# Kernel tuning notes

Hardware: AMD Instinct MI355X
Metric: run time of the kernel (lower is better)

## Reference

```python
import jax, jax.numpy as jnp
import numpy as np

EPS = 1e-05


def setup_inputs() -> dict:
    key = jax.random.key(0)
    k1, k2, k3, k4, k5 = jax.random.split(key, 5)
    B, Cin, T = 8, 512, 4096
    K, N, D = 8, 2048, 256
    return {
        "embeddings": jax.random.normal(k1, (B, Cin, T), dtype=jnp.float32),
        "w_in": jax.random.normal(k2, (D, Cin), dtype=jnp.float32) * 0.05,
        "w_out": jax.random.normal(k3, (Cin, D), dtype=jnp.float32) * 0.05,
        "embed_sum": jax.random.normal(k4, (K, N, D), dtype=jnp.float32),
        "cluster_usage": jax.random.uniform(k5, (K, N), dtype=jnp.float32, minval=0.5, maxval=1.5),
    }


def reference(embeddings, w_in, w_out, embed_sum, cluster_usage):
    # input_proj: 1x1 conv == channel matmul. [B, 512, T] -> [B, T, 256]
    x = jnp.einsum("dc,bct->btd", w_in, embeddings)
    # per-quantizer codebooks: embed_sum / clamp(cluster_usage)  -> [K, N, D]
    embeds = embed_sum / jnp.clip(cluster_usage, EPS, None)[..., None]

    def step(residual, embed):
        # squared-euclidean distance (same argmin as cdist p=2)
        # dists: [B, T, N]
        d = (
            jnp.sum(residual * residual, axis=-1, keepdims=True)
            - 2.0 * jnp.einsum("btd,nd->btn", residual, embed)
            + jnp.sum(embed * embed, axis=-1)
        )
        idx = jnp.argmin(d, axis=-1)          # [B, T] int
        q = embed[idx]                        # gather -> [B, T, D]
        return residual - q, (idx, q)

    _, (codes, qs) = jax.lax.scan(step, x, embeds)
    # codes: [K, B, T]; qs: [K, B, T, D]
    quantized = jnp.sum(qs, axis=0)           # decode: sum over quantizers
    out = jnp.einsum("cd,btd->bct", w_out, quantized)  # output_proj -> [B, 512, T]
    return codes, out
```

## Files before the change

kernel.cpp:

```cpp
#include <hip/hip_runtime.h>
#include <float.h>
#include <math.h>

#define EPSF 1e-5f
#define NRM_BIAS 2048.0f

constexpr int B_  = 8;
constexpr int CIN = 512;
constexpr int T_  = 4096;
constexpr int K_  = 8;
constexpr int N_  = 2048;
constexpr int D_  = 256;
constexpr int BT  = B_ * T_;

typedef _Float16 v8h __attribute__((ext_vector_type(8)));
typedef _Float16 v4h __attribute__((ext_vector_type(4)));
typedef float    v4f __attribute__((ext_vector_type(4)));

static __device__ __forceinline__ unsigned umn(unsigned a, unsigned b) { return a < b ? a : b; }
static __device__ __forceinline__ unsigned umx(unsigned a, unsigned b) { return a > b ? a : b; }

__global__ void __launch_bounds__(256) prep_kernel(const float* __restrict__ embed_sum,
                                                   const float* __restrict__ usage,
                                                   float* __restrict__ inv,
                                                   float* __restrict__ nrm,
                                                   _Float16* __restrict__ ehs) {
  int w    = threadIdx.x >> 6;
  int lane = threadIdx.x & 63;
  int kn   = blockIdx.x * 4 + w;
  int k    = kn >> 11, n = kn & (N_ - 1);
  const float* s = embed_sum + (size_t)kn * D_;
  float um = fmaxf(usage[kn], EPSF);
  float4 sv = *(const float4*)(s + lane * 4);
  float e0 = sv.x / um, e1 = sv.y / um, e2 = sv.z / um, e3 = sv.w / um;
  float v = e0 * e0 + e1 * e1 + e2 * e2 + e3 * e3;

  int half = n >> 10, chunk = (n >> 4) & 63, r = n & 15;
  int cg = lane >> 1, sub = lane & 1;
  v4h h4; h4[0] = (_Float16)e0; h4[1] = (_Float16)e1;
  h4[2] = (_Float16)e2; h4[3] = (_Float16)e3;
  size_t off16 = ((size_t)((k * 2 + half) * 64 + chunk)) * 4096
               + (size_t)(cg * 16 + r) * 8 + (size_t)sub * 4;
  *(v4h*)(ehs + off16) = h4;

  for (int off = 32; off > 0; off >>= 1) v += __shfl_down(v, off);
  if (lane == 0) { inv[kn] = 1.0f / um; nrm[kn] = v + NRM_BIAS; }
}

__global__ void __launch_bounds__(64) wprep_x_kernel(const float* __restrict__ w_in,
                                                     v8h* __restrict__ afragX) {
  int lane = threadIdx.x;
  int mt = blockIdx.x >> 4, kstep = blockIdx.x & 15;
  int m = mt * 16 + (lane & 15), k0 = kstep * 32 + (lane >> 4) * 8;
  const float* src = w_in + (size_t)m * CIN + k0;
  float4 f0 = *(const float4*)src, f1 = *(const float4*)(src + 4);
  float e[8] = {f0.x, f0.y, f0.z, f0.w, f1.x, f1.y, f1.z, f1.w};
  v8h h, l;
#pragma unroll
  for (int j = 0; j < 8; j++) {
    _Float16 hh = (_Float16)e[j];
    h[j] = hh; l[j] = (_Float16)(e[j] - (float)hh);
  }
  v8h* dst = afragX + ((size_t)blockIdx.x * 64 + lane) * 2;
  dst[0] = h; dst[1] = l;
}

__global__ void __launch_bounds__(256) wc_kernel(const float* __restrict__ w_out,
                                                 const float* __restrict__ w_in,
                                                 float* __restrict__ wc) {
  int c  = blockIdx.x >> 1;
  int cp = (blockIdx.x & 1) * 256 + threadIdx.x;
  float acc = 0.f;
  for (int d = 0; d < D_; d++)
    acc += w_out[(size_t)c * D_ + d] * w_in[(size_t)d * CIN + cp];
  wc[(size_t)c * CIN + cp] = acc;
}

__global__ void __launch_bounds__(64) wprep_o_kernel(const float* __restrict__ wc,
                                                     const float* __restrict__ w_out,
                                                     v8h* __restrict__ afragO) {
  int lane = threadIdx.x;
  int mt = blockIdx.x / 24, kstep = blockIdx.x % 24;
  int m = mt * 16 + (lane & 15), k0 = kstep * 32 + (lane >> 4) * 8;
  float e[8];
  if (k0 < CIN) {
    const float* s = wc + (size_t)m * CIN + k0;
#pragma unroll
    for (int j = 0; j < 8; j++) e[j] = s[j];
  } else {
    const float* s = w_out + (size_t)m * D_ + (k0 - CIN);
#pragma unroll
    for (int j = 0; j < 8; j++) e[j] = -s[j];
  }
  v8h h, l;
#pragma unroll
  for (int j = 0; j < 8; j++) {
    _Float16 hh = (_Float16)e[j];
    h[j] = hh; l[j] = (_Float16)(e[j] - (float)hh);
  }
  v8h* dst = afragO + ((size_t)blockIdx.x * 64 + lane) * 2;
  dst[0] = h; dst[1] = l;
}

__global__ void __launch_bounds__(256, 4) proj_x_kernel(const float* __restrict__ emb,
                                                        const v8h* __restrict__ afragX,
                                                        float* __restrict__ rb) {
  int tid = threadIdx.x, wave = tid >> 6, lane = tid & 63;
  int lr = lane & 15, lg = lane >> 4;
  int tb = blockIdx.x >> 1, nb = blockIdx.x & 1;
  int t0 = tb * 64 + wave * 16;
  int b  = t0 >> 12;
  const float* ebase = emb + (size_t)b * CIN * T_ + (t0 & (T_ - 1)) + lr;

  v4f acc[8];
#pragma unroll
  for (int nt = 0; nt < 8; nt++) acc[nt] = (v4f){0.f, 0.f, 0.f, 0.f};

  for (int ks = 0; ks < 16; ks++) {
    float e[8];
#pragma unroll
    for (int j = 0; j < 8; j++)
      e[j] = ebase[(size_t)(ks * 32 + lg * 8 + j) * T_];
    v8h Eh, El;
#pragma unroll
    for (int j = 0; j < 8; j++) {
      _Float16 hh = (_Float16)e[j];
      Eh[j] = hh; El[j] = (_Float16)(e[j] - (float)hh);
    }
    const v8h* ap = afragX + ((size_t)ks * 64 + lane) * 2;
#pragma unroll
    for (int nt = 0; nt < 8; nt++) {
      int mt = nb * 8 + nt;
      v8h Wh = ap[(size_t)mt * 2048];
      v8h Wl = ap[(size_t)mt * 2048 + 1];
      acc[nt] = __builtin_amdgcn_mfma_f32_16x16x32_f16(Eh, Wh, acc[nt], 0, 0, 0);
      acc[nt] = __builtin_amdgcn_mfma_f32_16x16x32_f16(El, Wh, acc[nt], 0, 0, 0);
      acc[nt] = __builtin_amdgcn_mfma_f32_16x16x32_f16(Eh, Wl, acc[nt], 0, 0, 0);
    }
  }
#pragma unroll
  for (int nt = 0; nt < 8; nt++)
#pragma unroll
    for (int r = 0; r < 4; r++)
      rb[(size_t)(t0 + lg * 4 + r) * D_ + (nb * 8 + nt) * 16 + lr] = acc[nt][r];
}

__global__ void __launch_bounds__(256, 4) proj_out_kernel(const float* __restrict__ emb,
                                                          const float* __restrict__ rb,
                                                          const v8h* __restrict__ afragO,
                                                          float* __restrict__ outb) {
  int tid = threadIdx.x, wave = tid >> 6, lane = tid & 63;
  int lr = lane & 15, lg = lane >> 4;
  int tb = blockIdx.x >> 1, mb = blockIdx.x & 1;
  int t0 = tb * 64 + wave * 16;
  int b  = t0 >> 12;
  const float* ebase = emb + (size_t)b * CIN * T_ + (t0 & (T_ - 1)) + lr;

  v4f acc[16];
#pragma unroll
  for (int mt = 0; mt < 16; mt++) acc[mt] = (v4f){0.f, 0.f, 0.f, 0.f};

  for (int ks = 0; ks < 24; ks++) {
    float e[8];
    if (ks < 16) {
#pragma unroll
      for (int j = 0; j < 8; j++)
        e[j] = ebase[(size_t)(ks * 32 + lg * 8 + j) * T_];
    } else {
      const float* rrow = rb + (size_t)(t0 + lr) * D_ + (ks - 16) * 32 + lg * 8;
      float4 f0 = *(const float4*)rrow, f1 = *(const float4*)(rrow + 4);
      e[0] = f0.x; e[1] = f0.y; e[2] = f0.z; e[3] = f0.w;
      e[4] = f1.x; e[5] = f1.y; e[6] = f1.z; e[7] = f1.w;
    }
    v8h Bh;
#pragma unroll
    for (int j = 0; j < 8; j++) Bh[j] = (_Float16)e[j];
#pragma unroll
    for (int mt = 0; mt < 16; mt++) {
      v8h Ah = afragO[(((size_t)(mb * 16 + mt) * 24 + ks) * 64 + lane) * 2];
      acc[mt] = __builtin_amdgcn_mfma_f32_16x16x32_f16(Ah, Bh, acc[mt], 0, 0, 0);
    }
  }
  float* op = outb + (size_t)b * CIN * T_ + (t0 & (T_ - 1)) + lr;
#pragma unroll
  for (int mt = 0; mt < 16; mt++)
#pragma unroll
    for (int r = 0; r < 4; r++)
      op[(size_t)((mb * 16 + mt) * 16 + lg * 4 + r) * T_] = acc[mt][r];
}

__device__ __forceinline__ void merge_save(unsigned b1[4], unsigned b2[4], unsigned b3[4],
                                           int half, int wave, int lg, int lr,
                                           int (*candL)[6]) {
#pragma unroll
  for (int rI = 0; rI < 4; rI++) {
    unsigned k1 = b1[rI], k2 = b2[rI], k3 = b3[rI];
    int n1 = (int)(k1 & 127u) * 16 + lr;
    int n2 = (int)(k2 & 127u) * 16 + lr;
    int n3 = (int)(k3 & 127u) * 16 + lr;
    int o0 = 0, o1 = 0, o2v = 0;
#pragma unroll
    for (int round = 0; round < 3; round++) {
      unsigned mk = k1; int mn = n1;
#pragma unroll
      for (int st = 1; st < 16; st <<= 1) {
        unsigned ok = (unsigned)__shfl_xor((int)mk, st);
        int      on = __shfl_xor(mn, st);
        bool t = (ok < mk) || (ok == mk && on < mn);
        mk = t ? ok : mk; mn = t ? on : mn;
      }
      if (round == 0) o0 = mn; else if (round == 1) o1 = mn; else o2v = mn;
      bool own = (k1 == mk) && (n1 == mn);
      k1 = own ? k2 : k1; n1 = own ? n2 : n1;
      k2 = own ? k3 : k2; n2 = own ? n3 : n2;
      k3 = own ? 0xFFFFFFFFu : k3; n3 = own ? 0x7fffffff : n3;
    }
    if (lr == 0) {
      int* cp = candL[wave * 16 + lg * 4 + rI] + half * 3;
      cp[0] = o0; cp[1] = o1; cp[2] = o2v;
    }
  }
}

__global__ void __launch_bounds__(512) rvq_fused_kernel(const _Float16* __restrict__ ehs,
                                                        const float* __restrict__ nrm,
                                                        const float* __restrict__ inv_,
                                                        const float* __restrict__ usage,
                                                        const float* __restrict__ embed_sum,
                                                        float* __restrict__ rb,
                                                        float* __restrict__ codes_f, int k) {
  __shared__ v8h ldsB[2][1024];
  __shared__ int candL[128][6];

  int tid  = threadIdx.x;
  int wave = tid >> 6, lane = tid & 63;
  int lr = lane & 15, lg = lane >> 4;
  int wbase = blockIdx.x * 128 + wave * 16;

  v8h A[8];
  {
    const float* rrow = rb + (size_t)(wbase + lr) * D_;
#pragma unroll
    for (int c = 0; c < 8; c++) {
      int k0 = c * 32 + lg * 8;
      float4 f0 = *(const float4*)(rrow + k0);
      float4 f1 = *(const float4*)(rrow + k0 + 4);
      v8h a;
      a[0] = (_Float16)f0.x; a[1] = (_Float16)f0.y;
      a[2] = (_Float16)f0.z; a[3] = (_Float16)f0.w;
      a[4] = (_Float16)f1.x; a[5] = (_Float16)f1.y;
      a[6] = (_Float16)f1.z; a[7] = (_Float16)f1.w;
      A[c] = a;
    }
  }

  const v8h* src = (const v8h*)(ehs + (size_t)k * 2 * (64 * 4096));
  ldsB[0][tid]       = src[tid];
  ldsB[0][512 + tid] = src[512 + tid];

  unsigned b1[4], b2[4], b3[4];
#pragma unroll
  for (int i = 0; i < 4; i++) { b1[i] = b2[i] = b3[i] = 0xFFFFFFFFu; }
  const float* nrm_k = nrm + (size_t)k * N_;
  __syncthreads();

  for (int p = 0; p < 64; p++) {
    int cur = p & 1;
    v8h nxt0, nxt1;
    bool more = (p + 1 < 64);
    if (more) {
      nxt0 = src[(size_t)(p + 1) * 1024 + tid];
      nxt1 = src[(size_t)(p + 1) * 1024 + 512 + tid];
    }

    v4f accA = {0.f, 0.f, 0.f, 0.f}, accB = {0.f, 0.f, 0.f, 0.f};
#pragma unroll
    for (int c = 0; c < 8; c++) {
      v8h BfA = ldsB[cur][(c * 4 + lg) * 16 + lr];
      v8h BfB = ldsB[cur][512 + (c * 4 + lg) * 16 + lr];
      accA = __builtin_amdgcn_mfma_f32_16x16x32_f16(A[c], BfA, accA, 0, 0, 0);
      accB = __builtin_amdgcn_mfma_f32_16x16x32_f16(A[c], BfB, accB, 0, 0, 0);
    }
    unsigned cgA = 2 * p, cgB = 2 * p + 1;
    float nvA = nrm_k[cgA * 16 + lr];
    float nvB = nrm_k[cgB * 16 + lr];
#pragma unroll
    for (int j = 0; j < 4; j++) {
      {
        float s = fmaf(-2.0f, accA[j], nvA);
        unsigned pk = (__float_as_uint(s) & 0xFFFFFF80u) | cgA;
        unsigned t = umx(b1[j], pk);
        unsigned u = umx(b2[j], pk);
        b1[j] = umn(b1[j], pk);
        b2[j] = umn(b2[j], t);
        b3[j] = umn(b3[j], u);
      }
      {
        float s = fmaf(-2.0f, accB[j], nvB);
        unsigned pk = (__float_as_uint(s) & 0xFFFFFF80u) | cgB;
        unsigned t = umx(b1[j], pk);
        unsigned u = umx(b2[j], pk);
        b1[j] = umn(b1[j], pk);
        b2[j] = umn(b2[j], t);
        b3[j] = umn(b3[j], u);
      }
    }
    if (more) {
      ldsB[cur ^ 1][tid]       = nxt0;
      ldsB[cur ^ 1][512 + tid] = nxt1;
    }
    if (p == 31) {
      merge_save(b1, b2, b3, 0, wave, lg, lr, candL);
#pragma unroll
      for (int i = 0; i < 4; i++) { b1[i] = b2[i] = b3[i] = 0xFFFFFFFFu; }
    }
    __syncthreads();
  }
  merge_save(b1, b2, b3, 1, wave, lg, lr, candL);
  __syncthreads();

  int tt = tid >> 2, q = tid & 3;
  int token = blockIdx.x * 128 + tt;
  const float* es_k  = embed_sum + (size_t)k * N_ * D_;
  const float* us_k  = usage + (size_t)k * N_;
  const float* inv_k = inv_  + (size_t)k * N_;

  int c6[6];
#pragma unroll
  for (int i = 0; i < 6; i++) c6[i] = candL[tt][i];
  float* rrow = rb + (size_t)token * D_;
  float* rq = rrow + q * 64;
  float4 rv[16];
#pragma unroll
  for (int m = 0; m < 16; m++) rv[m] = *(const float4*)(rq + m * 4);

  float dots[6];
#pragma unroll
  for (int i = 0; i < 6; i++) {
    const float* sr = es_k + (size_t)c6[i] * D_ + q * 64;
    float a = 0.f;
#pragma unroll
    for (int m = 0; m < 16; m++) {
      float4 sv = *(const float4*)(sr + m * 4);
      a += rv[m].x * sv.x + rv[m].y * sv.y + rv[m].z * sv.z + rv[m].w * sv.w;
    }
    dots[i] = a;
  }
#pragma unroll
  for (int st = 1; st < 4; st <<= 1) {
#pragma unroll
    for (int i = 0; i < 6; i++) dots[i] += __shfl_xor(dots[i], st);
  }

  float bs = FLT_MAX, bv2 = FLT_MAX; int bn = 0x7fffffff, bn2 = 0x7fffffff;
#pragma unroll
  for (int i = 0; i < 6; i++) {
    int n = c6[i];
    float s = nrm_k[n] - 2.0f * inv_k[n] * dots[i];
    bool better = (s < bs) || (s == bs && n < bn);
    bool second = (s < bv2) || (s == bv2 && n < bn2);
    if (better)      { bv2 = bs; bn2 = bn; bs = s; bn = n; }
    else if (second) { bv2 = s;  bn2 = n; }
  }
  int winner = bn;
  if (bv2 - bs < 0.5f && bn2 != bn) {
    double sc[2]; int nn[2] = { bn, bn2 };
#pragma unroll
    for (int cI = 0; cI < 2; cI++) {
      double u = fmax((double)us_k[nn[cI]], 1e-5);
      double uinv = 1.0 / u;
      const float* srow = es_k + (size_t)nn[cI] * D_ + q * 64;
      double dotre = 0.0, ee = 0.0;
#pragma unroll
      for (int m = 0; m < 16; m++) {
        float4 sv = *(const float4*)(srow + m * 4);
        double e0 = (double)sv.x * uinv, e1 = (double)sv.y * uinv;
        double e2 = (double)sv.z * uinv, e3 = (double)sv.w * uinv;
        dotre += (double)rv[m].x * e0 + (double)rv[m].y * e1
               + (double)rv[m].z * e2 + (double)rv[m].w * e3;
        ee += e0 * e0 + e1 * e1 + e2 * e2 + e3 * e3;
      }
      dotre += __shfl_xor(dotre, 1); dotre += __shfl_xor(dotre, 2);
      ee    += __shfl_xor(ee, 1);    ee    += __shfl_xor(ee, 2);
      sc[cI] = ee - 2.0 * dotre;
    }
    if (sc[1] < sc[0] || (sc[1] == sc[0] && nn[1] < nn[0])) winner = nn[1];
  }

  float um = fmaxf(us_k[winner], EPSF);
  const float* sw = es_k + (size_t)winner * D_ + q * 64;
#pragma unroll
  for (int m = 0; m < 16; m++) {
    float4 sv = *(const float4*)(sw + m * 4);
    rv[m].x -= sv.x / um; rv[m].y -= sv.y / um;
    rv[m].z -= sv.z / um; rv[m].w -= sv.w / um;
    *(float4*)(rq + m * 4) = rv[m];
  }
  if (q == 0) codes_f[(size_t)k * BT + token] = (float)winner;
}

extern "C" void kernel_launch(void* const* d_in, const int* in_sizes, int n_in,
                              void* d_out, int out_size, void* d_ws, size_t ws_size,
                              hipStream_t stream) {
  const float* emb       = (const float*)d_in[0];
  const float* w_in      = (const float*)d_in[1];
  const float* w_out     = (const float*)d_in[2];
  const float* embed_sum = (const float*)d_in[3];
  const float* usage     = (const float*)d_in[4];

  float* outp    = (float*)d_out;
  float* codes_f = outp;
  float* proj_o  = outp + (size_t)K_ * BT;

  float* rb   = (float*)d_ws;
  float* inv  = rb + (size_t)BT * D_;
  float* nrm  = inv + (size_t)K_ * N_;
  int*   cand = (int*)(nrm + (size_t)K_ * N_);
  _Float16* ehs = (_Float16*)(cand + (size_t)BT * 6);
  v8h* afragX = (v8h*)(ehs + (size_t)K_ * N_ * D_);
  float* wc   = (float*)(afragX + 16 * 16 * 64 * 2);
  v8h* afragO = (v8h*)(wc + 512 * 512);

  hipLaunchKernelGGL(wprep_x_kernel, dim3(256), dim3(64), 0, stream, w_in, afragX);
  hipLaunchKernelGGL(wc_kernel, dim3(1024), dim3(256), 0, stream, w_out, w_in, wc);
  hipLaunchKernelGGL(wprep_o_kernel, dim3(768), dim3(64), 0, stream, wc, w_out, afragO);
  hipLaunchKernelGGL(prep_kernel, dim3(K_ * N_ / 4), dim3(256), 0, stream,
                     embed_sum, usage, inv, nrm, ehs);
  hipLaunchKernelGGL(proj_x_kernel, dim3(BT / 32), dim3(256), 0, stream,
                     emb, afragX, rb);
  for (int k = 0; k < K_; k++)
    hipLaunchKernelGGL(rvq_fused_kernel, dim3(BT / 128), dim3(512), 0, stream,
                       ehs, nrm, inv, usage, embed_sum, rb, codes_f, k);
  hipLaunchKernelGGL(proj_out_kernel, dim3(BT / 32), dim3(256), 0, stream,
                     emb, rb, afragO, proj_o);
}
```

Before: 997.4 us.

## Fuse all eight quantizer stages into one kernel with register-resident residual

Replaces the eight per-quantizer launches with a single kernel that loops over quantizers, keeping each token's residual in registers (64 floats per lane) instead of reloading and storing it through global memory at every stage. The refinement and residual-update phase is remapped so that the same lanes that own the MFMA A-fragment own the residual slice, with cross-lane reductions over lane groups. The intent is to remove per-stage launch overhead and residual global-memory round trips. The cost is higher register pressure from the 64-float array, which the launch bound of two blocks per CU is meant to accommodate.

Measured after the change: 894.1 us. 1.12x faster.

```diff
diff --git a/kernel.cpp b/kernel.cpp
--- a/kernel.cpp
+++ b/kernel.cpp
@@ -222,13 +222,13 @@
   }
 }
 
-__global__ void __launch_bounds__(512) rvq_fused_kernel(const _Float16* __restrict__ ehs,
-                                                        const float* __restrict__ nrm,
-                                                        const float* __restrict__ inv_,
-                                                        const float* __restrict__ usage,
-                                                        const float* __restrict__ embed_sum,
-                                                        float* __restrict__ rb,
-                                                        float* __restrict__ codes_f, int k) {
+__global__ void __launch_bounds__(512, 2) rvq_mega_kernel(const _Float16* __restrict__ ehs,
+                                                          const float* __restrict__ nrm,
+                                                          const float* __restrict__ inv_,
+                                                          const float* __restrict__ usage,
+                                                          const float* __restrict__ embed_sum,
+                                                          float* __restrict__ rb,
+                                                          float* __restrict__ codes_f) {
   __shared__ v8h ldsB[2][1024];
   __shared__ int candL[128][6];
 
@@ -236,167 +236,194 @@
   int wave = tid >> 6, lane = tid & 63;
   int lr = lane & 15, lg = lane >> 4;
   int wbase = blockIdx.x * 128 + wave * 16;
-
-  v8h A[8];
+  int token = wbase + lr;
+
+  float r64[64];
   {
-    const float* rrow = rb + (size_t)(wbase + lr) * D_;
+    const float* rrow = rb + (size_t)token * D_ + lg * 8;
 #pragma unroll
     for (int c = 0; c < 8; c++) {
-      int k0 = c * 32 + lg * 8;
-      float4 f0 = *(const float4*)(rrow + k0);
-      float4 f1 = *(const float4*)(rrow + k0 + 4);
+      float4 f0 = *(const float4*)(rrow + c * 32);
+      float4 f1 = *(const float4*)(rrow + c * 32 + 4);
+      r64[c * 8 + 0] = f0.x; r64[c * 8 + 1] = f0.y;
+      r64[c * 8 + 2] = f0.z; r64[c * 8 + 3] = f0.w;
+      r64[c * 8 + 4] = f1.x; r64[c * 8 + 5] = f1.y;
+      r64[c * 8 + 6] = f1.z; r64[c * 8 + 7] = f1.w;
+    }
+  }
+
+  for (int k = 0; k < K_; k++) {
+    v8h A[8];
+#pragma unroll
+    for (int c = 0; c < 8; c++) {
       v8h a;
-      a[0] = (_Float16)f0.x; a[1] = (_Float16)f0.y;
-      a[2] = (_Float16)f0.z; a[3] = (_Float16)f0.w;
-      a[4] = (_Float16)f1.x; a[5] = (_Float16)f1.y;
-      a[6] = (_Float16)f1.z; a[7] = (_Float16)f1.w;
+#pragma unroll
+      for (int j = 0; j < 8; j++) a[j] = (_Float16)r64[c * 8 + j];
       A[c] = a;
     }
-  }
-
-  const v8h* src = (const v8h*)(ehs + (size_t)k * 2 * (64 * 4096));
-  ldsB[0][tid]       = src[tid];
-  ldsB[0][512 + tid] = src[512 + tid];
-
-  unsigned b1[4], b2[4], b3[4];
-#pragma unroll
-  for (int i = 0; i < 4; i++) { b1[i] = b2[i] = b3[i] = 0xFFFFFFFFu; }
-  const float* nrm_k = nrm + (size_t)k * N_;
-  __syncthreads();
-
-  for (int p = 0; p < 64; p++) {
-    int cur = p & 1;
-    v8h nxt0, nxt1;
-    bool more = (p + 1 < 64);
-    if (more) {
-      nxt0 = src[(size_t)(p + 1) * 1024 + tid];
-      nxt1 = src[(size_t)(p + 1) * 1024 + 512 + tid];
-    }
-
-    v4f accA = {0.f, 0.f, 0.f, 0.f}, accB = {0.f, 0.f, 0.f, 0.f};
+
+    const v8h* src = (const v8h*)(ehs + (size_t)k * 2 * (64 * 4096));
+    ldsB[0][tid]       = src[tid];
+    ldsB[0][512 + tid] = src[512 + tid];
+
+    unsigned b1[4], b2[4], b3[4];
+#pragma unroll
+    for (int i = 0; i < 4; i++) { b1[i] = b2[i] = b3[i] = 0xFFFFFFFFu; }
+    const float* nrm_k = nrm + (size_t)k * N_;
+    __syncthreads();
+
+    for (int p = 0; p < 64; p++) {
+      int cur = p & 1;
+      v8h nxt0, nxt1;
+      bool more = (p + 1 < 64);
+      if (more) {
+        nxt0 = src[(size_t)(p + 1) * 1024 + tid];
+        nxt1 = src[(size_t)(p + 1) * 1024 + 512 + tid];
+      }
+
+      v4f accA = {0.f, 0.f, 0.f, 0.f}, accB = {0.f, 0.f, 0.f, 0.f};
+#pragma unroll
+      for (int c = 0; c < 8; c++) {
+        v8h BfA = ldsB[cur][(c * 4 + lg) * 16 + lr];
+        v8h BfB = ldsB[cur][512 + (c * 4 + lg) * 16 + lr];
+        accA = __builtin_amdgcn_mfma_f32_16x16x32_f16(A[c], BfA, accA, 0, 0, 0);
+        accB = __builtin_amdgcn_mfma_f32_16x16x32_f16(A[c], BfB, accB, 0, 0, 0);
+      }
+      unsigned cgA = 2 * p, cgB = 2 * p + 1;
+      float nvA = nrm_k[cgA * 16 + lr];
+      float nvB = nrm_k[cgB * 16 + lr];
+#pragma unroll
+      for (int j = 0; j < 4; j++) {
+        {
+          float s = fmaf(-2.0f, accA[j], nvA);
+          unsigned pk = (__float_as_uint(s) & 0xFFFFFF80u) | cgA;
+          unsigned t = umx(b1[j], pk);
+          unsigned u = umx(b2[j], pk);
+          b1[j] = umn(b1[j], pk);
+          b2[j] = umn(b2[j], t);
+          b3[j] = umn(b3[j], u);
+        }
+        {
+          float s = fmaf(-2.0f, accB[j], nvB);
+          unsigned pk = (__float_as_uint(s) & 0xFFFFFF80u) | cgB;
+          unsigned t = umx(b1[j], pk);
+          unsigned u = umx(b2[j], pk);
+          b1[j] = umn(b1[j], pk);
+          b2[j] = umn(b2[j], t);
+          b3[j] = umn(b3[j], u);
+        }
+      }
+      if (more) {
+        ldsB[cur ^ 1][tid]       = nxt0;
+        ldsB[cur ^ 1][512 + tid] = nxt1;
+      }
+      if (p == 31) {
+        merge_save(b1, b2, b3, 0, wave, lg, lr, candL);
+#pragma unroll
+        for (int i = 0; i < 4; i++) { b1[i] = b2[i] = b3[i] = 0xFFFFFFFFu; }
+      }
+      __syncthreads();
+    }
+    merge_save(b1, b2, b3, 1, wave, lg, lr, candL);
+    __syncthreads();
+
+    const float* es_k  = embed_sum + (size_t)k * N_ * D_;
+    const float* us_k  = usage + (size_t)k * N_;
+    const float* inv_k = inv_  + (size_t)k * N_;
+
+    int c6[6];
+#pragma unroll
+    for (int i = 0; i < 6; i++) c6[i] = candL[wave * 16 + lr][i];
+
+    float dots[6];
+#pragma unroll
+    for (int i = 0; i < 6; i++) {
+      const float* sr = es_k + (size_t)c6[i] * D_ + lg * 8;
+      float a = 0.f;
+#pragma unroll
+      for (int c = 0; c < 8; c++) {
+        float4 s0 = *(const float4*)(sr + c * 32);
+        float4 s1 = *(const float4*)(sr + c * 32 + 4);
+        a += r64[c * 8 + 0] * s0.x + r64[c * 8 + 1] * s0.y
+           + r64[c * 8 + 2] * s0.z + r64[c * 8 + 3] * s0.w
+           + r64[c * 8 + 4] * s1.x + r64[c * 8 + 5] * s1.y
+           + r64[c * 8 + 6] * s1.z + r64[c * 8 + 7] * s1.w;
+      }
+      dots[i] = a;
+    }
+#pragma unroll
+    for (int i = 0; i < 6; i++) {
+      dots[i] += __shfl_xor(dots[i], 16);
+      dots[i] += __shfl_xor(dots[i], 32);
+    }
+
+    float bs = FLT_MAX, bv2 = FLT_MAX; int bn = 0x7fffffff, bn2 = 0x7fffffff;
+#pragma unroll
+    for (int i = 0; i < 6; i++) {
+      int n = c6[i];
+      float s = nrm_k[n] - 2.0f * inv_k[n] * dots[i];
+      bool better = (s < bs) || (s == bs && n < bn);
+      bool second = (s < bv2) || (s == bv2 && n < bn2);
+      if (better)      { bv2 = bs; bn2 = bn; bs = s; bn = n; }
+      else if (second) { bv2 = s;  bn2 = n; }
+    }
+    int winner = bn;
+    if (bv2 - bs < 0.5f && bn2 != bn) {
+      double sc[2]; int nn[2] = { bn, bn2 };
+#pragma unroll
+      for (int cI = 0; cI < 2; cI++) {
+        double u = fmax((double)us_k[nn[cI]], 1e-5);
+        double uinv = 1.0 / u;
+        const float* srow = es_k + (size_t)nn[cI] * D_ + lg * 8;
+        double dotre = 0.0, ee = 0.0;
+#pragma unroll
+        for (int c = 0; c < 8; c++) {
+          float4 s0 = *(const float4*)(srow + c * 32);
+          float4 s1 = *(const float4*)(srow + c * 32 + 4);
+          double e0 = (double)s0.x * uinv, e1 = (double)s0.y * uinv;
+          double e2 = (double)s0.z * uinv, e3 = (double)s0.w * uinv;
+          double e4 = (double)s1.x * uinv, e5 = (double)s1.y * uinv;
+          double e6 = (double)s1.z * uinv, e7 = (double)s1.w * uinv;
+          dotre += (double)r64[c * 8 + 0] * e0 + (double)r64[c * 8 + 1] * e1
+                 + (double)r64[c * 8 + 2] * e2 + (double)r64[c * 8 + 3] * e3
+                 + (double)r64[c * 8 + 4] * e4 + (double)r64[c * 8 + 5] * e5
+                 + (double)r64[c * 8 + 6] * e6 + (double)r64[c * 8 + 7] * e7;
+          ee += e0 * e0 + e1 * e1 + e2 * e2 + e3 * e3
+              + e4 * e4 + e5 * e5 + e6 * e6 + e7 * e7;
+        }
+        dotre += __shfl_xor(dotre, 16); dotre += __shfl_xor(dotre, 32);
+        ee    += __shfl_xor(ee, 16);    ee    += __shfl_xor(ee, 32);
+        sc[cI] = ee - 2.0 * dotre;
+      }
+      if (sc[1] < sc[0] || (sc[1] == sc[0] && nn[1] < nn[0])) winner = nn[1];
+    }
+
+    float um = fmaxf(us_k[winner], EPSF);
+    const float* sw = es_k + (size_t)winner * D_ + lg * 8;
 #pragma unroll
     for (int c = 0; c < 8; c++) {
-      v8h BfA = ldsB[cur][(c * 4 + lg) * 16 + lr];
-      v8h BfB = ldsB[cur][512 + (c * 4 + lg) * 16 + lr];
-      accA = __builtin_amdgcn_mfma_f32_16x16x32_f16(A[c], BfA, accA, 0, 0, 0);
-      accB = __builtin_amdgcn_mfma_f32_16x16x32_f16(A[c], BfB, accB, 0, 0, 0);
-    }
-    unsigned cgA = 2 * p, cgB = 2 * p + 1;
-    float nvA = nrm_k[cgA * 16 + lr];
-    float nvB = nrm_k[cgB * 16 + lr];
-#pragma unroll
-    for (int j = 0; j < 4; j++) {
-      {
-        float s = fmaf(-2.0f, accA[j], nvA);
-        unsigned pk = (__float_as_uint(s) & 0xFFFFFF80u) | cgA;
-        unsigned t = umx(b1[j], pk);
-        unsigned u = umx(b2[j], pk);
-        b1[j] = umn(b1[j], pk);
-        b2[j] = umn(b2[j], t);
-        b3[j] = umn(b3[j], u);
-      }
-      {
-        float s = fmaf(-2.0f, accB[j], nvB);
-        unsigned pk = (__float_as_uint(s) & 0xFFFFFF80u) | cgB;
-        unsigned t = umx(b1[j], pk);
-        unsigned u = umx(b2[j], pk);
-        b1[j] = umn(b1[j], pk);
-        b2[j] = umn(b2[j], t);
-        b3[j] = umn(b3[j], u);
-      }
-    }
-    if (more) {
-      ldsB[cur ^ 1][tid]       = nxt0;
-      ldsB[cur ^ 1][512 + tid] = nxt1;
-    }
-    if (p == 31) {
-      merge_save(b1, b2, b3, 0, wave, lg, lr, candL);
-#pragma unroll
-      for (int i = 0; i < 4; i++) { b1[i] = b2[i] = b3[i] = 0xFFFFFFFFu; }
-    }
-    __syncthreads();
-  }
-  merge_save(b1, b2, b3, 1, wave, lg, lr, candL);
-  __syncthreads();
-
-  int tt = tid >> 2, q = tid & 3;
-  int token = blockIdx.x * 128 + tt;
-  const float* es_k  = embed_sum + (size_t)k * N_ * D_;
-  const float* us_k  = usage + (size_t)k * N_;
-  const float* inv_k = inv_  + (size_t)k * N_;
-
-  int c6[6];
-#pragma unroll
-  for (int i = 0; i < 6; i++) c6[i] = candL[tt][i];
-  float* rrow = rb + (size_t)token * D_;
-  float* rq = rrow + q * 64;
-  float4 rv[16];
-#pragma unroll
-  for (int m = 0; m < 16; m++) rv[m] = *(const float4*)(rq + m * 4);
-
-  float dots[6];
-#pragma unroll
-  for (int i = 0; i < 6; i++) {
-    const float* sr = es_k + (size_t)c6[i] * D_ + q * 64;
-    float a = 0.f;
-#pragma unroll
-    for (int m = 0; m < 16; m++) {
-      float4 sv = *(const float4*)(sr + m * 4);
-      a += rv[m].x * sv.x + rv[m].y * sv.y + rv[m].z * sv.z + rv[m].w * sv.w;
-    }
-    dots[i] = a;
-  }
-#pragma unroll
-  for (int st = 1; st < 4; st <<= 1) {
-#pragma unroll
-    for (int i = 0; i < 6; i++) dots[i] += __shfl_xor(dots[i], st);
-  }
-
-  float bs = FLT_MAX, bv2 = FLT_MAX; int bn = 0x7fffffff, bn2 = 0x7fffffff;
-#pragma unroll
-  for (int i = 0; i < 6; i++) {
-    int n = c6[i];
-    float s = nrm_k[n] - 2.0f * inv_k[n] * dots[i];
-    bool better = (s < bs) || (s == bs && n < bn);
-    bool second = (s < bv2) || (s == bv2 && n < bn2);
-    if (better)      { bv2 = bs; bn2 = bn; bs = s; bn = n; }
-    else if (second) { bv2 = s;  bn2 = n; }
-  }
-  int winner = bn;
-  if (bv2 - bs < 0.5f && bn2 != bn) {
-    double sc[2]; int nn[2] = { bn, bn2 };
-#pragma unroll
-    for (int cI = 0; cI < 2; cI++) {
-      double u = fmax((double)us_k[nn[cI]], 1e-5);
-      double uinv = 1.0 / u;
-      const float* srow = es_k + (size_t)nn[cI] * D_ + q * 64;
-      double dotre = 0.0, ee = 0.0;
-#pragma unroll
-      for (int m = 0; m < 16; m++) {
-        float4 sv = *(const float4*)(srow + m * 4);
-        double e0 = (double)sv.x * uinv, e1 = (double)sv.y * uinv;
-        double e2 = (double)sv.z * uinv, e3 = (double)sv.w * uinv;
-        dotre += (double)rv[m].x * e0 + (double)rv[m].y * e1
-               + (double)rv[m].z * e2 + (double)rv[m].w * e3;
-        ee += e0 * e0 + e1 * e1 + e2 * e2 + e3 * e3;
-      }
-      dotre += __shfl_xor(dotre, 1); dotre += __shfl_xor(dotre, 2);
-      ee    += __shfl_xor(ee, 1);    ee    += __shfl_xor(ee, 2);
-      sc[cI] = ee - 2.0 * dotre;
-    }
-    if (sc[1] < sc[0] || (sc[1] == sc[0] && nn[1] < nn[0])) winner = nn[1];
-  }
-
-  float um = fmaxf(us_k[winner], EPSF);
-  const float* sw = es_k + (size_t)winner * D_ + q * 64;
-#pragma unroll
-  for (int m = 0; m < 16; m++) {
-    float4 sv = *(const float4*)(sw + m * 4);
-    rv[m].x -= sv.x / um; rv[m].y -= sv.y / um;
-    rv[m].z -= sv.z / um; rv[m].w -= sv.w / um;
-    *(float4*)(rq + m * 4) = rv[m];
-  }
-  if (q == 0) codes_f[(size_t)k * BT + token] = (float)winner;
+      float4 s0 = *(const float4*)(sw + c * 32);
+      float4 s1 = *(const float4*)(sw + c * 32 + 4);
+      r64[c * 8 + 0] -= s0.x / um; r64[c * 8 + 1] -= s0.y / um;
+      r64[c * 8 + 2] -= s0.z / um; r64[c * 8 + 3] -= s0.w / um;
+      r64[c * 8 + 4] -= s1.x / um; r64[c * 8 + 5] -= s1.y / um;
+      r64[c * 8 + 6] -= s1.z / um; r64[c * 8 + 7] -= s1.w / um;
+    }
+    if (lg == 0) codes_f[(size_t)k * BT + token] = (float)winner;
+  }
+
+  {
+    float* wrow = rb + (size_t)token * D_ + lg * 8;
+#pragma unroll
+    for (int c = 0; c < 8; c++) {
+      float4 f0 = make_float4(r64[c * 8 + 0], r64[c * 8 + 1],
+                              r64[c * 8 + 2], r64[c * 8 + 3]);
+      float4 f1 = make_float4(r64[c * 8 + 4], r64[c * 8 + 5],
+                              r64[c * 8 + 6], r64[c * 8 + 7]);
+      *(float4*)(wrow + c * 32)     = f0;
+      *(float4*)(wrow + c * 32 + 4) = f1;
+    }
+  }
 }
 
 extern "C" void kernel_launch(void* const* d_in, const int* in_sizes, int n_in,
@@ -428,9 +455,8 @@
                      embed_sum, usage, inv, nrm, ehs);
   hipLaunchKernelGGL(proj_x_kernel, dim3(BT / 32), dim3(256), 0, stream,
                      emb, afragX, rb);
-  for (int k = 0; k < K_; k++)
-    hipLaunchKernelGGL(rvq_fused_kernel, dim3(BT / 128), dim3(512), 0, stream,
-                       ehs, nrm, inv, usage, embed_sum, rb, codes_f, k);
+  hipLaunchKernelGGL(rvq_mega_kernel, dim3(BT / 128), dim3(512), 0, stream,
+                     ehs, nrm, inv, usage, embed_sum, rb, codes_f);
   hipLaunchKernelGGL(proj_out_kernel, dim3(BT / 32), dim3(256), 0, stream,
                      emb, rb, afragO, proj_o);
 }
```

## Fuse all quantizer stages into one persistent kernel with 32 tokens per wave

Applied to the files above, without the earlier changes.

Replaces the eight per-quantizer launches with a single kernel that loops over the quantizers. Each block still handles its own 128 tokens, and the residuals stay block-local from one stage to the next. Each wave now covers 32 tokens with two A-fragment sets, so every codebook tile read from LDS feeds twice as many MFMAs. Codebook tiles are staged with global_load_lds direct-to-LDS copies instead of register round-trips. The cost is half as many waves per block (256 threads), more registers for accumulators and top-3 lists, and a serial candidate-rescore phase done in two halves.

Measured after the change: 1.202 ms. 1.21x slower.

```diff
diff --git a/kernel.cpp b/kernel.cpp
--- a/kernel.cpp
+++ b/kernel.cpp
@@ -19,6 +19,15 @@
 
 static __device__ __forceinline__ unsigned umn(unsigned a, unsigned b) { return a < b ? a : b; }
 static __device__ __forceinline__ unsigned umx(unsigned a, unsigned b) { return a > b ? a : b; }
+
+static __device__ __forceinline__ void ins3(unsigned& B1, unsigned& B2, unsigned& B3,
+                                            unsigned pk) {
+  unsigned t = umx(B1, pk);
+  unsigned u = umx(B2, pk);
+  B1 = umn(B1, pk);
+  B2 = umn(B2, t);
+  B3 = umn(B3, u);
+}
 
 __global__ void __launch_bounds__(256) prep_kernel(const float* __restrict__ embed_sum,
                                                    const float* __restrict__ usage,
@@ -189,11 +198,11 @@
       op[(size_t)((mb * 16 + mt) * 16 + lg * 4 + r) * T_] = acc[mt][r];
 }
 
-__device__ __forceinline__ void merge_save(unsigned b1[4], unsigned b2[4], unsigned b3[4],
-                                           int half, int wave, int lg, int lr,
-                                           int (*candL)[6]) {
-#pragma unroll
-  for (int rI = 0; rI < 4; rI++) {
+__device__ __forceinline__ void merge_save8(unsigned b1[8], unsigned b2[8], unsigned b3[8],
+                                            int half, int wave, int lg, int lr,
+                                            int (*candL)[6]) {
+#pragma unroll
+  for (int rI = 0; rI < 8; rI++) {
     unsigned k1 = b1[rI], k2 = b2[rI], k3 = b3[rI];
     int n1 = (int)(k1 & 127u) * 16 + lr;
     int n2 = (int)(k2 & 127u) * 16 + lr;
@@ -216,187 +225,191 @@
       k3 = own ? 0xFFFFFFFFu : k3; n3 = own ? 0x7fffffff : n3;
     }
     if (lr == 0) {
-      int* cp = candL[wave * 16 + lg * 4 + rI] + half * 3;
+      int* cp = candL[wave * 32 + (rI >> 2) * 16 + lg * 4 + (rI & 3)] + half * 3;
       cp[0] = o0; cp[1] = o1; cp[2] = o2v;
     }
   }
 }
 
-__global__ void __launch_bounds__(512) rvq_fused_kernel(const _Float16* __restrict__ ehs,
-                                                        const float* __restrict__ nrm,
-                                                        const float* __restrict__ inv_,
-                                                        const float* __restrict__ usage,
-                                                        const float* __restrict__ embed_sum,
-                                                        float* __restrict__ rb,
-                                                        float* __restrict__ codes_f, int k) {
+__global__ void __launch_bounds__(256) rvq_mega_kernel(const _Float16* __restrict__ ehs,
+                                                       const float* __restrict__ nrm,
+                                                       const float* __restrict__ inv_,
+                                                       const float* __restrict__ usage,
+                                                       const float* __restrict__ embed_sum,
+                                                       float* __restrict__ rb,
+                                                       float* __restrict__ codes_f) {
   __shared__ v8h ldsB[2][1024];
   __shared__ int candL[128][6];
 
   int tid  = threadIdx.x;
   int wave = tid >> 6, lane = tid & 63;
   int lr = lane & 15, lg = lane >> 4;
-  int wbase = blockIdx.x * 128 + wave * 16;
-
-  v8h A[8];
-  {
-    const float* rrow = rb + (size_t)(wbase + lr) * D_;
-#pragma unroll
-    for (int c = 0; c < 8; c++) {
-      int k0 = c * 32 + lg * 8;
-      float4 f0 = *(const float4*)(rrow + k0);
-      float4 f1 = *(const float4*)(rrow + k0 + 4);
-      v8h a;
-      a[0] = (_Float16)f0.x; a[1] = (_Float16)f0.y;
-      a[2] = (_Float16)f0.z; a[3] = (_Float16)f0.w;
-      a[4] = (_Float16)f1.x; a[5] = (_Float16)f1.y;
-      a[6] = (_Float16)f1.z; a[7] = (_Float16)f1.w;
-      A[c] = a;
-    }
-  }
-
-  const v8h* src = (const v8h*)(ehs + (size_t)k * 2 * (64 * 4096));
-  ldsB[0][tid]       = src[tid];
-  ldsB[0][512 + tid] = src[512 + tid];
-
-  unsigned b1[4], b2[4], b3[4];
-#pragma unroll
-  for (int i = 0; i < 4; i++) { b1[i] = b2[i] = b3[i] = 0xFFFFFFFFu; }
-  const float* nrm_k = nrm + (size_t)k * N_;
-  __syncthreads();
-
-  for (int p = 0; p < 64; p++) {
-    int cur = p & 1;
-    v8h nxt0, nxt1;
-    bool more = (p + 1 < 64);
-    if (more) {
-      nxt0 = src[(size_t)(p + 1) * 1024 + tid];
-      nxt1 = src[(size_t)(p + 1) * 1024 + 512 + tid];
-    }
-
-    v4f accA = {0.f, 0.f, 0.f, 0.f}, accB = {0.f, 0.f, 0.f, 0.f};
-#pragma unroll
-    for (int c = 0; c < 8; c++) {
-      v8h BfA = ldsB[cur][(c * 4 + lg) * 16 + lr];
-      v8h BfB = ldsB[cur][512 + (c * 4 + lg) * 16 + lr];
-      accA = __builtin_amdgcn_mfma_f32_16x16x32_f16(A[c], BfA, accA, 0, 0, 0);
-      accB = __builtin_amdgcn_mfma_f32_16x16x32_f16(A[c], BfB, accB, 0, 0, 0);
-    }
-    unsigned cgA = 2 * p, cgB = 2 * p + 1;
-    float nvA = nrm_k[cgA * 16 + lr];
-    float nvB = nrm_k[cgB * 16 + lr];
-#pragma unroll
-    for (int j = 0; j < 4; j++) {
-      {
-        float s = fmaf(-2.0f, accA[j], nvA);
-        unsigned pk = (__float_as_uint(s) & 0xFFFFFF80u) | cgA;
-        unsigned t = umx(b1[j], pk);
-        unsigned u = umx(b2[j], pk);
-        b1[j] = umn(b1[j], pk);
-        b2[j] = umn(b2[j], t);
-        b3[j] = umn(b3[j], u);
-      }
-      {
-        float s = fmaf(-2.0f, accB[j], nvB);
-        unsigned pk = (__float_as_uint(s) & 0xFFFFFF80u) | cgB;
-        unsigned t = umx(b1[j], pk);
-        unsigned u = umx(b2[j], pk);
-        b1[j] = umn(b1[j], pk);
-        b2[j] = umn(b2[j], t);
-        b3[j] = umn(b3[j], u);
-      }
-    }
-    if (more) {
-      ldsB[cur ^ 1][tid]       = nxt0;
-      ldsB[cur ^ 1][512 + tid] = nxt1;
-    }
-    if (p == 31) {
-      merge_save(b1, b2, b3, 0, wave, lg, lr, candL);
-#pragma unroll
-      for (int i = 0; i < 4; i++) { b1[i] = b2[i] = b3[i] = 0xFFFFFFFFu; }
-    }
+  int wbase = blockIdx.x * 128 + wave * 32;
+
+  for (int k = 0; k < K_; k++) {
+    v8h A[2][8];
+#pragma unroll
+    for (int tau = 0; tau < 2; tau++) {
+      const float* rrow = rb + (size_t)(wbase + tau * 16 + lr) * D_ + lg * 8;
+#pragma unroll
+      for (int c = 0; c < 8; c++) {
+        float4 f0 = *(const float4*)(rrow + c * 32);
+        float4 f1 = *(const float4*)(rrow + c * 32 + 4);
+        v8h a;
+        a[0] = (_Float16)f0.x; a[1] = (_Float16)f0.y;
+        a[2] = (_Float16)f0.z; a[3] = (_Float16)f0.w;
+        a[4] = (_Float16)f1.x; a[5] = (_Float16)f1.y;
+        a[6] = (_Float16)f1.z; a[7] = (_Float16)f1.w;
+        A[tau][c] = a;
+      }
+    }
+
+    const v8h* src = (const v8h*)(ehs + (size_t)k * 2 * (64 * 4096));
+
+#pragma unroll
+    for (int q = 0; q < 4; q++) {
+      int idx = tid + q * 256;
+      __builtin_amdgcn_global_load_lds(
+          (__attribute__((address_space(1))) void*)(void*)(src + idx),
+          (__attribute__((address_space(3))) void*)(&ldsB[0][idx]), 16, 0, 0);
+    }
+
+    unsigned b1[8], b2[8], b3[8];
+#pragma unroll
+    for (int i = 0; i < 8; i++) { b1[i] = b2[i] = b3[i] = 0xFFFFFFFFu; }
+    const float* nrm_k = nrm + (size_t)k * N_;
     __syncthreads();
-  }
-  merge_save(b1, b2, b3, 1, wave, lg, lr, candL);
-  __syncthreads();
-
-  int tt = tid >> 2, q = tid & 3;
-  int token = blockIdx.x * 128 + tt;
-  const float* es_k  = embed_sum + (size_t)k * N_ * D_;
-  const float* us_k  = usage + (size_t)k * N_;
-  const float* inv_k = inv_  + (size_t)k * N_;
-
-  int c6[6];
-#pragma unroll
-  for (int i = 0; i < 6; i++) c6[i] = candL[tt][i];
-  float* rrow = rb + (size_t)token * D_;
-  float* rq = rrow + q * 64;
-  float4 rv[16];
-#pragma unroll
-  for (int m = 0; m < 16; m++) rv[m] = *(const float4*)(rq + m * 4);
-
-  float dots[6];
-#pragma unroll
-  for (int i = 0; i < 6; i++) {
-    const float* sr = es_k + (size_t)c6[i] * D_ + q * 64;
-    float a = 0.f;
-#pragma unroll
-    for (int m = 0; m < 16; m++) {
-      float4 sv = *(const float4*)(sr + m * 4);
-      a += rv[m].x * sv.x + rv[m].y * sv.y + rv[m].z * sv.z + rv[m].w * sv.w;
-    }
-    dots[i] = a;
-  }
-#pragma unroll
-  for (int st = 1; st < 4; st <<= 1) {
-#pragma unroll
-    for (int i = 0; i < 6; i++) dots[i] += __shfl_xor(dots[i], st);
-  }
-
-  float bs = FLT_MAX, bv2 = FLT_MAX; int bn = 0x7fffffff, bn2 = 0x7fffffff;
-#pragma unroll
-  for (int i = 0; i < 6; i++) {
-    int n = c6[i];
-    float s = nrm_k[n] - 2.0f * inv_k[n] * dots[i];
-    bool better = (s < bs) || (s == bs && n < bn);
-    bool second = (s < bv2) || (s == bv2 && n < bn2);
-    if (better)      { bv2 = bs; bn2 = bn; bs = s; bn = n; }
-    else if (second) { bv2 = s;  bn2 = n; }
-  }
-  int winner = bn;
-  if (bv2 - bs < 0.5f && bn2 != bn) {
-    double sc[2]; int nn[2] = { bn, bn2 };
-#pragma unroll
-    for (int cI = 0; cI < 2; cI++) {
-      double u = fmax((double)us_k[nn[cI]], 1e-5);
-      double uinv = 1.0 / u;
-      const float* srow = es_k + (size_t)nn[cI] * D_ + q * 64;
-      double dotre = 0.0, ee = 0.0;
+
+    for (int p = 0; p < 64; p++) {
+      int cur = p & 1;
+      if (p + 1 < 64) {
+        const v8h* gsrc = src + (size_t)(p + 1) * 1024;
+#pragma unroll
+        for (int q = 0; q < 4; q++) {
+          int idx = tid + q * 256;
+          __builtin_amdgcn_global_load_lds(
+              (__attribute__((address_space(1))) void*)(void*)(gsrc + idx),
+              (__attribute__((address_space(3))) void*)(&ldsB[cur ^ 1][idx]), 16, 0, 0);
+        }
+      }
+
+      v4f a0A = {0,0,0,0}, a0B = {0,0,0,0}, a1A = {0,0,0,0}, a1B = {0,0,0,0};
+#pragma unroll
+      for (int c = 0; c < 8; c++) {
+        v8h BfA = ldsB[cur][(c * 4 + lg) * 16 + lr];
+        v8h BfB = ldsB[cur][512 + (c * 4 + lg) * 16 + lr];
+        a0A = __builtin_amdgcn_mfma_f32_16x16x32_f16(A[0][c], BfA, a0A, 0, 0, 0);
+        a0B = __builtin_amdgcn_mfma_f32_16x16x32_f16(A[0][c], BfB, a0B, 0, 0, 0);
+        a1A = __builtin_amdgcn_mfma_f32_16x16x32_f16(A[1][c], BfA, a1A, 0, 0, 0);
+        a1B = __builtin_amdgcn_mfma_f32_16x16x32_f16(A[1][c], BfB, a1B, 0, 0, 0);
+      }
+      unsigned cgA = 2 * p, cgB = 2 * p + 1;
+      float nvA = nrm_k[cgA * 16 + lr];
+      float nvB = nrm_k[cgB * 16 + lr];
+#pragma unroll
+      for (int j = 0; j < 4; j++) {
+        float s0A = fmaf(-2.0f, a0A[j], nvA);
+        ins3(b1[j], b2[j], b3[j], (__float_as_uint(s0A) & 0xFFFFFF80u) | cgA);
+        float s0B = fmaf(-2.0f, a0B[j], nvB);
+        ins3(b1[j], b2[j], b3[j], (__float_as_uint(s0B) & 0xFFFFFF80u) | cgB);
+        float s1A = fmaf(-2.0f, a1A[j], nvA);
+        ins3(b1[4 + j], b2[4 + j], b3[4 + j], (__float_as_uint(s1A) & 0xFFFFFF80u) | cgA);
+        float s1B = fmaf(-2.0f, a1B[j], nvB);
+        ins3(b1[4 + j], b2[4 + j], b3[4 + j], (__float_as_uint(s1B) & 0xFFFFFF80u) | cgB);
+      }
+      if (p == 31) {
+        merge_save8(b1, b2, b3, 0, wave, lg, lr, candL);
+#pragma unroll
+        for (int i = 0; i < 8; i++) { b1[i] = b2[i] = b3[i] = 0xFFFFFFFFu; }
+      }
+      __syncthreads();
+    }
+    merge_save8(b1, b2, b3, 1, wave, lg, lr, candL);
+    __syncthreads();
+
+    const float* es_k  = embed_sum + (size_t)k * N_ * D_;
+    const float* us_k  = usage + (size_t)k * N_;
+    const float* inv_k = inv_  + (size_t)k * N_;
+
+    for (int h = 0; h < 2; h++) {
+      int tt = h * 64 + (tid >> 2), q = tid & 3;
+      int token = blockIdx.x * 128 + tt;
+
+      int c6[6];
+#pragma unroll
+      for (int i = 0; i < 6; i++) c6[i] = candL[tt][i];
+      float* rrow = rb + (size_t)token * D_;
+      float* rq = rrow + q * 64;
+      float4 rv[16];
+#pragma unroll
+      for (int m = 0; m < 16; m++) rv[m] = *(const float4*)(rq + m * 4);
+
+      float dots[6];
+#pragma unroll
+      for (int i = 0; i < 6; i++) {
+        const float* sr = es_k + (size_t)c6[i] * D_ + q * 64;
+        float a = 0.f;
+#pragma unroll
+        for (int m = 0; m < 16; m++) {
+          float4 sv = *(const float4*)(sr + m * 4);
+          a += rv[m].x * sv.x + rv[m].y * sv.y + rv[m].z * sv.z + rv[m].w * sv.w;
+        }
+        dots[i] = a;
+      }
+#pragma unroll
+      for (int st = 1; st < 4; st <<= 1) {
+#pragma unroll
+        for (int i = 0; i < 6; i++) dots[i] += __shfl_xor(dots[i], st);
+      }
+
+      float bs = FLT_MAX, bv2 = FLT_MAX; int bn = 0x7fffffff, bn2 = 0x7fffffff;
+#pragma unroll
+      for (int i = 0; i < 6; i++) {
+        int n = c6[i];
+        float s = nrm_k[n] - 2.0f * inv_k[n] * dots[i];
+        bool better = (s < bs) || (s == bs && n < bn);
+        bool second = (s < bv2) || (s == bv2 && n < bn2);
+        if (better)      { bv2 = bs; bn2 = bn; bs = s; bn = n; }
+        else if (second) { bv2 = s;  bn2 = n; }
+      }
+      int winner = bn;
+      if (bv2 - bs < 0.5f && bn2 != bn) {
+        double sc[2]; int nn[2] = { bn, bn2 };
+#pragma unroll
+        for (int cI = 0; cI < 2; cI++) {
+          double u = fmax((double)us_k[nn[cI]], 1e-5);
+          double uinv = 1.0 / u;
+          const float* srow = es_k + (size_t)nn[cI] * D_ + q * 64;
+          double dotre = 0.0, ee = 0.0;
+#pragma unroll
+          for (int m = 0; m < 16; m++) {
+            float4 sv = *(const float4*)(srow + m * 4);
+            double e0 = (double)sv.x * uinv, e1 = (double)sv.y * uinv;
+            double e2 = (double)sv.z * uinv, e3 = (double)sv.w * uinv;
+            dotre += (double)rv[m].x * e0 + (double)rv[m].y * e1
+                   + (double)rv[m].z * e2 + (double)rv[m].w * e3;
+            ee += e0 * e0 + e1 * e1 + e2 * e2 + e3 * e3;
+          }
+          dotre += __shfl_xor(dotre, 1); dotre += __shfl_xor(dotre, 2);
+          ee    += __shfl_xor(ee, 1);    ee    += __shfl_xor(ee, 2);
+          sc[cI] = ee - 2.0 * dotre;
+        }
+        if (sc[1] < sc[0] || (sc[1] == sc[0] && nn[1] < nn[0])) winner = nn[1];
+      }
+
+      float um = fmaxf(us_k[winner], EPSF);
+      const float* sw = es_k + (size_t)winner * D_ + q * 64;
 #pragma unroll
       for (int m = 0; m < 16; m++) {
-        float4 sv = *(const float4*)(srow + m * 4);
-        double e0 = (double)sv.x * uinv, e1 = (double)sv.y * uinv;
-        double e2 = (double)sv.z * uinv, e3 = (double)sv.w * uinv;
-        dotre += (double)rv[m].x * e0 + (double)rv[m].y * e1
-               + (double)rv[m].z * e2 + (double)rv[m].w * e3;
-        ee += e0 * e0 + e1 * e1 + e2 * e2 + e3 * e3;
-      }
-      dotre += __shfl_xor(dotre, 1); dotre += __shfl_xor(dotre, 2);
-      ee    += __shfl_xor(ee, 1);    ee    += __shfl_xor(ee, 2);
-      sc[cI] = ee - 2.0 * dotre;
-    }
-    if (sc[1] < sc[0] || (sc[1] == sc[0] && nn[1] < nn[0])) winner = nn[1];
-  }
-
-  float um = fmaxf(us_k[winner], EPSF);
-  const float* sw = es_k + (size_t)winner * D_ + q * 64;
-#pragma unroll
-  for (int m = 0; m < 16; m++) {
-    float4 sv = *(const float4*)(sw + m * 4);
-    rv[m].x -= sv.x / um; rv[m].y -= sv.y / um;
-    rv[m].z -= sv.z / um; rv[m].w -= sv.w / um;
-    *(float4*)(rq + m * 4) = rv[m];
-  }
-  if (q == 0) codes_f[(size_t)k * BT + token] = (float)winner;
+        float4 sv = *(const float4*)(sw + m * 4);
+        rv[m].x -= sv.x / um; rv[m].y -= sv.y / um;
+        rv[m].z -= sv.z / um; rv[m].w -= sv.w / um;
+        *(float4*)(rq + m * 4) = rv[m];
+      }
+      if (q == 0) codes_f[(size_t)k * BT + token] = (float)winner;
+    }
+    __syncthreads();
+  }
 }
 
 extern "C" void kernel_launch(void* const* d_in, const int* in_sizes, int n_in,
@@ -428,9 +441,8 @@
                      embed_sum, usage, inv, nrm, ehs);
   hipLaunchKernelGGL(proj_x_kernel, dim3(BT / 32), dim3(256), 0, stream,
                      emb, afragX, rb);
-  for (int k = 0; k < K_; k++)
-    hipLaunchKernelGGL(rvq_fused_kernel, dim3(BT / 128), dim3(512), 0, stream,
-                       ehs, nrm, inv, usage, embed_sum, rb, codes_f, k);
+  hipLaunchKernelGGL(rvq_mega_kernel, dim3(BT / 128), dim3(256), 0, stream,
+                     ehs, nrm, inv, usage, embed_sum, rb, codes_f);
   hipLaunchKernelGGL(proj_out_kernel, dim3(BT / 32), dim3(256), 0, stream,
                      emb, rb, afragO, proj_o);
 }
```
